# Performance work log

Hardware: AMD Instinct MI355X
Metric: run time of the kernel (lower is better)

## Reference

```python
import jax, jax.numpy as jnp
import numpy as np

B, S, LEN = 1024, 64, 48          # batch, max atoms, atoms per molecule
N = B * LEN                        # total nodes = node_mask.sum()
E = 4 * N                          # edges (avg degree ~4)
D = 256                            # input_dim == hidden_dim == d_model == d_ff
H, HD = D // 8, 8                  # num_heads = hidden_dim // 8
L = 3                              # transformer layers
VOCAB = 65


def _ln(z, s, b):
    mu = z.mean(-1, keepdims=True)
    var = ((z - mu) ** 2).mean(-1, keepdims=True)
    return (z - mu) * jax.lax.rsqrt(var + 1e-5) * s + b


def _forward(x_atoms, edge_index, node_mask, emb_table, conv1_w, conv1_b,
             conv2_w, conv2_b, in_w, in_b, attn_w, attn_b, proj_w, proj_b,
             ln1_s, ln1_b, ff1_w, ff1_b, ff2_w, ff2_b, ln2_s, ln2_b):
    n = x_atoms.shape[0]
    src, dst = edge_index[0], edge_index[1]
    # Embedding with max_norm=1 (torch renormalizes accessed rows)
    e = emb_table[x_atoms]
    nrm = jnp.linalg.norm(e, axis=-1, keepdims=True)
    e = e * jnp.minimum(1.0, 1.0 / (nrm + 1e-7))
    # GCN symmetric normalization with self-loops (shared by both convs)
    deg = jax.ops.segment_sum(jnp.ones((src.shape[0],), e.dtype), dst, num_segments=n) + 1.0
    dinv = jax.lax.rsqrt(deg)
    coef = (dinv[src] * dinv[dst])[:, None]       # per-edge norm
    self_coef = (dinv * dinv)[:, None]            # self-loop norm

    def gcn(h, W, b):
        h = h @ W
        agg = jax.ops.segment_sum(h[src] * coef, dst, num_segments=n)
        return agg + h * self_coef + b

    ones = jnp.ones((n, 1), e.dtype)
    pe = jax.nn.relu(gcn(ones, conv1_w, conv1_b))
    pe = gcn(pe, conv2_w, conv2_b)
    x = e + pe
    # masked_scatter into padded [B, S, D] (row-major fill order)
    mflat = node_mask.reshape(-1)
    rank = jnp.clip(jnp.cumsum(mflat) - 1, 0, n - 1)
    padded = jnp.where(mflat[:, None], x[rank], 0.0).reshape(B, S, D)
    # transformer encoder, post-LN, ReLU FFN; mask [B,1,S,1] as in original
    h = padded @ in_w + in_b
    qmask = node_mask[:, None, :, None]
    scale = 1.0 / np.sqrt(HD).astype(np.float32)
    for l in range(L):
        qkv = h @ attn_w[l] + attn_b[l]
        q, k, v = jnp.split(qkv, 3, axis=-1)
        q = q.reshape(B, S, H, HD)
        k = k.reshape(B, S, H, HD)
        v = v.reshape(B, S, H, HD)
        scores = jnp.einsum('bqhd,bkhd->bhqk', q, k) * scale
        scores = jnp.where(qmask, scores, -1e9)
        attn = jax.nn.softmax(scores, axis=-1)
        o = jnp.einsum('bhqk,bkhd->bqhd', attn, v).reshape(B, S, D)
        h = _ln(h + o @ proj_w[l] + proj_b[l], ln1_s[l], ln1_b[l])
        ff = jax.nn.relu(h @ ff1_w[l] + ff1_b[l]) @ ff2_w[l] + ff2_b[l]
        h = _ln(h + ff, ln2_s[l], ln2_b[l])
    return h


def setup_inputs() -> dict:
    key = jax.random.key(0)
    ks = jax.random.split(key, 16)
    x_atoms = jax.random.randint(ks[0], (N,), 0, VOCAB)
    edge_index = jax.random.randint(ks[1], (2, E), 0, N)
    node_mask = jnp.broadcast_to(jnp.arange(S)[None, :] < LEN, (B, S))
    f32 = jnp.float32
    p = lambda k, shp: (jax.random.normal(k, shp, f32) * 0.02)
    return {
        'x_atoms': x_atoms, 'edge_index': edge_index, 'node_mask': node_mask,
        'emb_table': jax.random.normal(ks[2], (VOCAB, D), f32),
        'conv1_w': p(ks[3], (1, D)), 'conv1_b': jnp.zeros((D,), f32),
        'conv2_w': p(ks[4], (D, D)), 'conv2_b': jnp.zeros((D,), f32),
        'in_w': p(ks[5], (D, D)), 'in_b': jnp.zeros((D,), f32),
        'attn_w': p(ks[6], (L, D, 3 * D)), 'attn_b': jnp.zeros((L, 3 * D), f32),
        'proj_w': p(ks[7], (L, D, D)), 'proj_b': jnp.zeros((L, D), f32),
        'ln1_s': jnp.ones((L, D), f32), 'ln1_b': jnp.zeros((L, D), f32),
        'ff1_w': p(ks[8], (L, D, D)), 'ff1_b': jnp.zeros((L, D), f32),
        'ff2_w': p(ks[9], (L, D, D)), 'ff2_b': jnp.zeros((L, D), f32),
        'ln2_s': jnp.ones((L, D), f32), 'ln2_b': jnp.zeros((L, D), f32),
    }


def reference(x_atoms, edge_index, node_mask, emb_table, conv1_w, conv1_b,
              conv2_w, conv2_b, in_w, in_b, attn_w, attn_b, proj_w, proj_b,
              ln1_s, ln1_b, ff1_w, ff1_b, ff2_w, ff2_b, ln2_s, ln2_b):
    return _forward(x_atoms, edge_index, node_mask, emb_table, conv1_w, conv1_b,
                    conv2_w, conv2_b, in_w, in_b, attn_w, attn_b, proj_w, proj_b,
                    ln1_s, ln1_b, ff1_w, ff1_b, ff2_w, ff2_b, ln2_s, ln2_b)
```

## Files before the change

kernel.cpp:

```cpp
#include <hip/hip_runtime.h>
#include <cstdint>
#include <cstddef>

#define B_   1024
#define S_   64
#define LEN_ 48
#define NN   (B_*LEN_)
#define EE   (4*NN)
#define D_   256
#define H_   32
#define HD_  8
#define ROWS (B_*S_)
#define PLANE 16777216

typedef float  f32x4  __attribute__((ext_vector_type(4)));
typedef __bf16 bf16x8 __attribute__((ext_vector_type(8)));

#define AS1(p) ((const __attribute__((address_space(1))) void*)(p))
#define AS3(p) ((__attribute__((address_space(3))) void*)(p))

__device__ __forceinline__ unsigned short f2bf(float f) {
    union { float f; unsigned u; } x; x.f = f;
    unsigned r = x.u + 0x7fffu + ((x.u >> 16) & 1u);
    return (unsigned short)(r >> 16);
}
__device__ __forceinline__ float bf2f(unsigned short h) {
    union { unsigned u; float f; } x; x.u = (unsigned)h << 16; return x.f;
}
__device__ __forceinline__ bf16x8 u4_to_bf8(uint4 u) {
    union { uint4 u; bf16x8 v; } c; c.u = u; return c.v;
}

__global__ void embed_kernel(const int* __restrict__ atoms,
                             const float* __restrict__ table,
                             float* __restrict__ e) {
    int wave = threadIdx.x >> 6, lane = threadIdx.x & 63;
    int row  = blockIdx.x * 4 + wave;
    int a    = atoms[row];
    float4 v = ((const float4*)(table + (size_t)a * D_))[lane];
    float ss = v.x*v.x + v.y*v.y + v.z*v.z + v.w*v.w;
    #pragma unroll
    for (int off = 32; off; off >>= 1) ss += __shfl_xor(ss, off);
    float nrm = sqrtf(ss);
    float sc  = fminf(1.0f, 1.0f / (nrm + 1e-7f));
    v.x *= sc; v.y *= sc; v.z *= sc; v.w *= sc;
    ((float4*)(e + (size_t)row * D_))[lane] = v;
}

__global__ void fill_kernel(const int* __restrict__ ei, int* __restrict__ cur,
                            int* __restrict__ bucket) {
    int e = blockIdx.x * 256 + threadIdx.x;
    if (e < EE) {
        int s = ei[e], d = ei[EE + e];
        int pos = atomicAdd(&cur[d], 1);
        if (pos < 32) bucket[d * 32 + pos] = s;
    }
}

__global__ void dinv_kernel(const int* __restrict__ cur, float* __restrict__ dinv) {
    int i = blockIdx.x * 256 + threadIdx.x;
    if (i < NN) dinv[i] = rsqrtf((float)cur[i] + 1.0f);
}

__global__ void agg1_kernel(const int* __restrict__ ei, const float* __restrict__ dinv,
                            float* __restrict__ agg1) {
    int e = blockIdx.x * 256 + threadIdx.x;
    if (e < EE) {
        int s = ei[e], d = ei[EE + e];
        atomicAdd(&agg1[d], dinv[s] * dinv[d]);
    }
}

__global__ void pe1_kernel(const float* __restrict__ agg1, const float* __restrict__ dinv,
                           const float* __restrict__ w1, const float* __restrict__ b1,
                           unsigned short* __restrict__ pe1) {
    size_t idx = (size_t)blockIdx.x * 256 + threadIdx.x;
    int i = (int)(idx >> 8), d = (int)(idx & 255);
    float c = agg1[i] + dinv[i] * dinv[i];
    pe1[idx] = f2bf(fmaxf(0.0f, w1[d] * c + b1[d]));
}

__global__ void wconv_kernel(const float* __restrict__ conv2_w, const float* __restrict__ in_w,
                             const float* __restrict__ attn_w, const float* __restrict__ proj_w,
                             const float* __restrict__ ff1_w, const float* __restrict__ ff2_w,
                             unsigned short* __restrict__ wt) {
    int z = blockIdx.y;
    int n = blockIdx.x, k = threadIdx.x;
    const float* src; unsigned short* dst; int N = 256;
    if      (z == 0) { src = conv2_w;                       dst = wt; }
    else if (z == 1) { src = in_w;                          dst = wt + 65536; }
    else if (z <  5) { int l = z - 2;  src = attn_w + (size_t)l * 196608; dst = wt + 131072  + (size_t)l * 196608; N = 768; }
    else if (z <  8) { int l = z - 5;  src = proj_w + (size_t)l * 65536;  dst = wt + 720896  + (size_t)l * 65536; }
    else if (z < 11) { int l = z - 8;  src = ff1_w  + (size_t)l * 65536;  dst = wt + 917504  + (size_t)l * 65536; }
    else             { int l = z - 11; src = ff2_w  + (size_t)l * 65536;  dst = wt + 1114112 + (size_t)l * 65536; }
    if (n < N) dst[(size_t)n * 256 + k] = f2bf(src[(size_t)k * N + n]);
}

__global__ __launch_bounds__(256) void gemm2(
        const unsigned short* __restrict__ A, const unsigned short* __restrict__ WT,
        const float* __restrict__ bias, unsigned short* __restrict__ C0,
        float* __restrict__ Cf, const unsigned short* __restrict__ zeros,
        int amode, int cmode, int relu) {
    __shared__ unsigned short As[128 * 64];
    __shared__ unsigned short Ws[128 * 64];
    const int t = threadIdx.x, w = t >> 6, lane = t & 63;
    const int lr = lane & 15, lq = lane >> 4;
    const size_t m0 = (size_t)blockIdx.y * 128;
    const int    n0 = blockIdx.x * 128;
    const int    N  = gridDim.x * 128;
    const int    wr = (w >> 1) * 64, wc = (w & 1) * 64;

    f32x4 acc[4][4];
    #pragma unroll
    for (int mi = 0; mi < 4; mi++)
        #pragma unroll
        for (int tt = 0; tt < 4; tt++) acc[mi][tt] = (f32x4){0.f, 0.f, 0.f, 0.f};

    const int srow = w * 32 + (lane >> 3);
    const int sj   = lane & 7;

    for (int ki = 0; ki < 4; ki++) {
        if (ki) __syncthreads();
        #pragma unroll
        for (int c = 0; c < 4; c++) {
            int row = srow + c * 8;
            {
                int gch = sj ^ (row & 7);
                const unsigned short* g;
                if (amode == 0) {
                    g = A + (m0 + row) * 256 + ki * 64 + gch * 8;
                } else {
                    size_t grow = m0 + row;
                    int s = (int)(grow & 63);
                    g = (s < LEN_) ? (A + ((grow >> 6) * LEN_ + s) * 256 + ki * 64 + gch * 8)
                                   : zeros;
                }
                __builtin_amdgcn_global_load_lds(AS1(g), AS3(As + w * 2048 + c * 512), 16, 0, 0);
            }
            {
                int gch = sj ^ (row & 7);
                const unsigned short* g = WT + (size_t)(n0 + row) * 256 + ki * 64 + gch * 8;
                __builtin_amdgcn_global_load_lds(AS1(g), AS3(Ws + w * 2048 + c * 512), 16, 0, 0);
            }
        }
        __syncthreads();
        #pragma unroll
        for (int ks = 0; ks < 2; ks++) {
            bf16x8 af[4], bf[4];
            #pragma unroll
            for (int mi = 0; mi < 4; mi++) {
                int row = wr + mi * 16 + lr;
                int cs = (ks * 4 + lq) ^ (row & 7);
                af[mi] = *(const bf16x8*)&As[row * 64 + cs * 8];
            }
            #pragma unroll
            for (int tt = 0; tt < 4; tt++) {
                int col = wc + tt * 16 + lr;
                int cs = (ks * 4 + lq) ^ (col & 7);
                bf[tt] = *(const bf16x8*)&Ws[col * 64 + cs * 8];
            }
            #pragma unroll
            for (int mi = 0; mi < 4; mi++)
                #pragma unroll
                for (int tt = 0; tt < 4; tt++)
                    acc[mi][tt] = __builtin_amdgcn_mfma_f32_16x16x32_bf16(af[mi], bf[tt], acc[mi][tt], 0, 0, 0);
        }
    }
    #pragma unroll
    for (int tt = 0; tt < 4; tt++) {
        int c = n0 + wc + tt * 16 + lr;
        float bv = bias ? bias[c] : 0.0f;
        #pragma unroll
        for (int mi = 0; mi < 4; mi++) {
            #pragma unroll
            for (int r = 0; r < 4; r++) {
                size_t grow = m0 + wr + mi * 16 + lq * 4 + r;
                float v = acc[mi][tt][r] + bv;
                if (relu) v = fmaxf(v, 0.0f);
                if (cmode == 0) {
                    C0[grow * (size_t)N + c] = f2bf(v);
                } else if (cmode == 2) {
                    C0[grow * 256 + c] = f2bf(v);
                    Cf[grow * 256 + c] = v;
                } else {
                    int p = c >> 8, h = (c >> 3) & 31, d = c & 7;
                    size_t bb = grow >> 6, s = grow & 63;
                    C0[(size_t)p * PLANE + ((bb * 32 + h) * 64 + s) * 8 + d] = f2bf(v);
                }
            }
        }
    }
}

__global__ void gather_kernel(const float* __restrict__ xbuf, const unsigned short* __restrict__ h2,
                              const int* __restrict__ cur, const int* __restrict__ bucket,
                              const float* __restrict__ dinv, const float* __restrict__ b2,
                              unsigned short* __restrict__ xg) {
    int w = threadIdx.x >> 6, lane = threadIdx.x & 63;
    int i = blockIdx.x * 4 + w;
    float di = dinv[i];
    ushort4 hv = ((const ushort4*)(h2 + (size_t)i * D_))[lane];
    float4  xv = ((const float4*)(xbuf + (size_t)i * D_))[lane];
    float4  bv = ((const float4*)b2)[lane];
    float a0 = xv.x + bf2f(hv.x) * di * di + bv.x;
    float a1 = xv.y + bf2f(hv.y) * di * di + bv.y;
    float a2 = xv.z + bf2f(hv.z) * di * di + bv.z;
    float a3 = xv.w + bf2f(hv.w) * di * di + bv.w;
    int deg = min(cur[i], 32);
    for (int e = 0; e < deg; e++) {
        int s = bucket[i * 32 + e];
        float c = dinv[s] * di;
        ushort4 sv = ((const ushort4*)(h2 + (size_t)s * D_))[lane];
        a0 += bf2f(sv.x) * c;
        a1 += bf2f(sv.y) * c;
        a2 += bf2f(sv.z) * c;
        a3 += bf2f(sv.w) * c;
    }
    ushort4 out;
    out.x = f2bf(a0); out.y = f2bf(a1); out.z = f2bf(a2); out.w = f2bf(a3);
    ((ushort4*)(xg + (size_t)i * D_))[lane] = out;
}

__global__ __launch_bounds__(256) void attn3_kernel(const unsigned short* __restrict__ qkv,
                                                    unsigned short* __restrict__ o) {
    __shared__ unsigned short Pb[4][64 * 64];
    __shared__ unsigned short VTb[4][16 * 64];
    const int b = blockIdx.x;
    const int w = threadIdx.x >> 6, lane = threadIdx.x & 63;
    const int lr = lane & 15, lq = lane >> 4;
    unsigned short* Pw  = Pb[w];
    unsigned short* VTw = VTb[w];
    const uint4* Q4 = (const uint4*)qkv;
    const uint4* K4 = Q4 + PLANE / 8;
    const uint4* V4 = Q4 + 2 * (PLANE / 8);
    const float scale = 0.35355339059327373f;
    const bf16x8 zf = u4_to_bf8(make_uint4(0, 0, 0, 0));

    for (int hh = 0; hh < 8; hh++) {
        const int h = w * 8 + hh;
        const size_t hb = ((size_t)b * 32 + h) * 64;

        {
            uint4 vrow = V4[hb + lane];
            union { uint4 u; unsigned short s[8]; } vu; vu.u = vrow;
            int ch = lane >> 3, jj = lane & 7;
            #pragma unroll
            for (int d = 0; d < 8; d++)
                VTw[d * 64 + (ch ^ (d & 7)) * 8 + jj] = vu.s[d];
        }

        bf16x8 af[4], bf[4];
        #pragma unroll
        for (int mi = 0; mi < 4; mi++)
            af[mi] = (lq == 0) ? u4_to_bf8(Q4[hb + mi * 16 + lr]) : zf;
        #pragma unroll
        for (int ni = 0; ni < 4; ni++)
            bf[ni] = (lq == 0) ? u4_to_bf8(K4[hb + ni * 16 + lr]) : zf;
        f32x4 s[4][4];
        #pragma unroll
        for (int mi = 0; mi < 4; mi++)
            #pragma unroll
            for (int ni = 0; ni < 4; ni++)
                s[mi][ni] = __builtin_amdgcn_mfma_f32_16x16x32_bf16(
                    af[mi], bf[ni], (f32x4){0.f, 0.f, 0.f, 0.f}, 0, 0, 0);
        #pragma unroll
        for (int ni = 0; ni < 4; ni++) s[3][ni] = (f32x4){0.f, 0.f, 0.f, 0.f};

        #pragma unroll
        for (int mi = 0; mi < 4; mi++) {
            float mx[4], sm[4];
            #pragma unroll
            for (int r = 0; r < 4; r++)
                mx[r] = fmaxf(fmaxf(s[mi][0][r], s[mi][1][r]), fmaxf(s[mi][2][r], s[mi][3][r]));
            #pragma unroll
            for (int st = 1; st <= 8; st <<= 1)
                #pragma unroll
                for (int r = 0; r < 4; r++) mx[r] = fmaxf(mx[r], __shfl_xor(mx[r], st));
            #pragma unroll
            for (int ni = 0; ni < 4; ni++)
                #pragma unroll
                for (int r = 0; r < 4; r++)
                    s[mi][ni][r] = __expf((s[mi][ni][r] - mx[r]) * scale);
            #pragma unroll
            for (int r = 0; r < 4; r++)
                sm[r] = (s[mi][0][r] + s[mi][1][r]) + (s[mi][2][r] + s[mi][3][r]);
            #pragma unroll
            for (int st = 1; st <= 8; st <<= 1)
                #pragma unroll
                for (int r = 0; r < 4; r++) sm[r] += __shfl_xor(sm[r], st);
            #pragma unroll
            for (int r = 0; r < 4; r++) sm[r] = 1.0f / sm[r];
            #pragma unroll
            for (int ni = 0; ni < 4; ni++) {
                int ch = ni * 2 + (lr >> 3), jj = lr & 7;
                #pragma unroll
                for (int r = 0; r < 4; r++) {
                    int q = mi * 16 + lq * 4 + r;
                    Pw[q * 64 + (ch ^ (q & 7)) * 8 + jj] = f2bf(s[mi][ni][r] * sm[r]);
                }
            }
        }

        bf16x8 av[2];
        #pragma unroll
        for (int ks = 0; ks < 2; ks++) {
            int cs = (ks * 4 + lq) ^ (lr & 7);
            av[ks] = *(const bf16x8*)&VTw[lr * 64 + cs * 8];
        }
        #pragma unroll
        for (int ni = 0; ni < 4; ni++) {
            f32x4 oa = (f32x4){0.f, 0.f, 0.f, 0.f};
            #pragma unroll
            for (int ks = 0; ks < 2; ks++) {
                int q = ni * 16 + lr;
                int cs = (ks * 4 + lq) ^ (q & 7);
                bf16x8 pb = *(const bf16x8*)&Pw[q * 64 + cs * 8];
                oa = __builtin_amdgcn_mfma_f32_16x16x32_bf16(av[ks], pb, oa, 0, 0, 0);
            }
            if (lq < 2) {
                int q = ni * 16 + lr;
                ushort4 ov;
                ov.x = f2bf(oa[0]); ov.y = f2bf(oa[1]);
                ov.z = f2bf(oa[2]); ov.w = f2bf(oa[3]);
                *(ushort4*)(o + ((size_t)b * 64 + q) * 256 + h * 8 + lq * 4) = ov;
            }
        }
    }
}

__global__ void ln_kernel(const float* __restrict__ resid, const unsigned short* __restrict__ delta,
                          const float* __restrict__ g, const float* __restrict__ bb,
                          float* __restrict__ outF, unsigned short* __restrict__ outB) {
    int wave = threadIdx.x >> 6, lane = threadIdx.x & 63;
    size_t row = (size_t)blockIdx.x * 4 + wave;
    float4 z0 = ((const float4*)(resid + row * D_))[lane];
    ushort4 d0 = ((const ushort4*)(delta + row * D_))[lane];
    float4 z;
    z.x = z0.x + bf2f(d0.x); z.y = z0.y + bf2f(d0.y);
    z.z = z0.z + bf2f(d0.z); z.w = z0.w + bf2f(d0.w);
    float s1 = z.x + z.y + z.z + z.w;
    float s2 = z.x*z.x + z.y*z.y + z.z*z.z + z.w*z.w;
    #pragma unroll
    for (int off = 32; off; off >>= 1) {
        s1 += __shfl_xor(s1, off);
        s2 += __shfl_xor(s2, off);
    }
    float mu  = s1 * (1.0f / 256.0f);
    float var = s2 * (1.0f / 256.0f) - mu * mu;
    float rs  = rsqrtf(var + 1e-5f);
    float4 gg = ((const float4*)g)[lane];
    float4 bv = ((const float4*)bb)[lane];
    float4 r;
    r.x = (z.x - mu) * rs * gg.x + bv.x;
    r.y = (z.y - mu) * rs * gg.y + bv.y;
    r.z = (z.z - mu) * rs * gg.z + bv.z;
    r.w = (z.w - mu) * rs * gg.w + bv.w;
    ((float4*)(outF + row * D_))[lane] = r;
    if (outB) {
        ushort4 hB;
        hB.x = f2bf(r.x); hB.y = f2bf(r.y); hB.z = f2bf(r.z); hB.w = f2bf(r.w);
        ((ushort4*)(outB + row * D_))[lane] = hB;
    }
}

extern "C" void kernel_launch(void* const* d_in, const int* in_sizes, int n_in,
                              void* d_out, int out_size, void* d_ws, size_t ws_size,
                              hipStream_t stream) {
    const int*   x_atoms = (const int*)d_in[0];
    const int*   ei      = (const int*)d_in[1];
    const float* emb     = (const float*)d_in[3];
    const float* conv1_w = (const float*)d_in[4];
    const float* conv1_b = (const float*)d_in[5];
    const float* conv2_w = (const float*)d_in[6];
    const float* conv2_b = (const float*)d_in[7];
    const float* in_w    = (const float*)d_in[8];
    const float* in_b    = (const float*)d_in[9];
    const float* attn_w  = (const float*)d_in[10];
    const float* attn_b  = (const float*)d_in[11];
    const float* proj_w  = (const float*)d_in[12];
    const float* proj_b  = (const float*)d_in[13];
    const float* ln1_s   = (const float*)d_in[14];
    const float* ln1_b   = (const float*)d_in[15];
    const float* ff1_w   = (const float*)d_in[16];
    const float* ff1_b   = (const float*)d_in[17];
    const float* ff2_w   = (const float*)d_in[18];
    const float* ff2_b   = (const float*)d_in[19];
    const float* ln2_s   = (const float*)d_in[20];
    const float* ln2_b   = (const float*)d_in[21];

    char* ws = (char*)d_ws;
    float*          xbuf = (float*)         (ws + 0);
    unsigned short* pe1  = (unsigned short*)(ws + 50331648);
    unsigned short* xg   = (unsigned short*)(ws + 50331648);
    unsigned short* h2   = (unsigned short*)(ws + 75497472);
    unsigned short* Qp   = (unsigned short*)(ws + 0);
    unsigned short* t1   = (unsigned short*)(ws + 33554432);
    unsigned short* t1bf = (unsigned short*)(ws + 0);
    float*          hbuf = (float*)         (ws + 100663296);
    unsigned short* hbf  = (unsigned short*)(ws + 167772160);
    unsigned short* obuf = (unsigned short*)(ws + 167772160);
    int*            bucket=(int*)           (ws + 201326592);
    unsigned short* wt   = (unsigned short*)(ws + 207618048);
    int*            cur  = (int*)           (ws + 210239488);
    float*          dinv = (float*)         (ws + 210436096);
    float*          agg1 = (float*)         (ws + 210632704);
    unsigned short* zpage= (unsigned short*)(ws + 210829312);

    hipMemsetAsync(cur,   0, NN * 4, stream);
    hipMemsetAsync(agg1,  0, NN * 4, stream);
    hipMemsetAsync(zpage, 0, 256, stream);

    wconv_kernel<<<dim3(768, 14), 256, 0, stream>>>(conv2_w, in_w, attn_w, proj_w, ff1_w, ff2_w, wt);

    embed_kernel<<<NN / 4, 256, 0, stream>>>(x_atoms, emb, xbuf);
    fill_kernel<<<EE / 256, 256, 0, stream>>>(ei, cur, bucket);
    dinv_kernel<<<NN / 256, 256, 0, stream>>>(cur, dinv);
    agg1_kernel<<<EE / 256, 256, 0, stream>>>(ei, dinv, agg1);
    pe1_kernel<<<NN, 256, 0, stream>>>(agg1, dinv, conv1_w, conv1_b, pe1);
    gemm2<<<dim3(2, NN / 128), 256, 0, stream>>>(pe1, wt, nullptr, h2, nullptr, zpage, 0, 0, 0);
    gather_kernel<<<NN / 4, 256, 0, stream>>>(xbuf, h2, cur, bucket, dinv, conv2_b, xg);

    gemm2<<<dim3(2, ROWS / 128), 256, 0, stream>>>(xg, wt + 65536, in_b, hbf, hbuf, zpage, 1, 2, 0);

    for (int l = 0; l < 3; l++) {
        gemm2<<<dim3(6, ROWS / 128), 256, 0, stream>>>(
            hbf, wt + 131072 + (size_t)l * 196608, attn_b + (size_t)l * 768,
            Qp, nullptr, zpage, 0, 3, 0);
        attn3_kernel<<<B_, 256, 0, stream>>>(Qp, obuf);
        gemm2<<<dim3(2, ROWS / 128), 256, 0, stream>>>(
            obuf, wt + 720896 + (size_t)l * 65536, proj_b + (size_t)l * D_,
            t1, nullptr, zpage, 0, 0, 0);
        ln_kernel<<<ROWS / 4, 256, 0, stream>>>(
            hbuf, t1, ln1_s + (size_t)l * D_, ln1_b + (size_t)l * D_, hbuf, hbf);
        gemm2<<<dim3(2, ROWS / 128), 256, 0, stream>>>(
            hbf, wt + 917504 + (size_t)l * 65536, ff1_b + (size_t)l * D_,
            t1bf, nullptr, zpage, 0, 0, 1);
        gemm2<<<dim3(2, ROWS / 128), 256, 0, stream>>>(
            t1bf, wt + 1114112 + (size_t)l * 65536, ff2_b + (size_t)l * D_,
            t1, nullptr, zpage, 0, 0, 0);
        if (l == 2) {
            ln_kernel<<<ROWS / 4, 256, 0, stream>>>(
                hbuf, t1, ln2_s + (size_t)l * D_, ln2_b + (size_t)l * D_, (float*)d_out, nullptr);
        } else {
            ln_kernel<<<ROWS / 4, 256, 0, stream>>>(
                hbuf, t1, ln2_s + (size_t)l * D_, ln2_b + (size_t)l * D_, hbuf, hbf);
        }
    }
}
```

Baseline: 1.201 ms.

## Fuse proj+LayerNorm and FFN+LayerNorm kernels, stage GEMM epilogue through LDS

```diff
diff --git a/kernel.cpp b/kernel.cpp
--- a/kernel.cpp
+++ b/kernel.cpp
@@ -100,14 +100,17 @@
         const unsigned short* __restrict__ A, const unsigned short* __restrict__ WT,
         const float* __restrict__ bias, unsigned short* __restrict__ C0,
         float* __restrict__ Cf, const unsigned short* __restrict__ zeros,
-        int amode, int cmode, int relu) {
-    __shared__ unsigned short As[128 * 64];
-    __shared__ unsigned short Ws[128 * 64];
+        int mt, int amode, int cmode, int relu) {
+    __shared__ unsigned short sh[16384];
+    unsigned short* Asm = sh;
+    unsigned short* Wsm = sh + 8192;
     const int t = threadIdx.x, w = t >> 6, lane = t & 63;
     const int lr = lane & 15, lq = lane >> 4;
-    const size_t m0 = (size_t)blockIdx.y * 128;
-    const int    n0 = blockIdx.x * 128;
-    const int    N  = gridDim.x * 128;
+    const int by = blockIdx.x % mt;
+    const int bx = blockIdx.x / mt;
+    const size_t m0 = (size_t)by * 128;
+    const int    n0 = bx * 128;
+    const int    N  = (gridDim.x / mt) * 128;
     const int    wr = (w >> 1) * 64, wc = (w & 1) * 64;
 
     f32x4 acc[4][4];
@@ -135,58 +138,81 @@
                     g = (s < LEN_) ? (A + ((grow >> 6) * LEN_ + s) * 256 + ki * 64 + gch * 8)
                                    : zeros;
                 }
-                __builtin_amdgcn_global_load_lds(AS1(g), AS3(As + w * 2048 + c * 512), 16, 0, 0);
+                __builtin_amdgcn_global_load_lds(AS1(g), AS3(Asm + w * 2048 + c * 512), 16, 0, 0);
             }
             {
                 int gch = sj ^ (row & 7);
                 const unsigned short* g = WT + (size_t)(n0 + row) * 256 + ki * 64 + gch * 8;
-                __builtin_amdgcn_global_load_lds(AS1(g), AS3(Ws + w * 2048 + c * 512), 16, 0, 0);
+                __builtin_amdgcn_global_load_lds(AS1(g), AS3(Wsm + w * 2048 + c * 512), 16, 0, 0);
             }
         }
         __syncthreads();
         #pragma unroll
         for (int ks = 0; ks < 2; ks++) {
-            bf16x8 af[4], bf[4];
+            bf16x8 af[4], bfr[4];
             #pragma unroll
             for (int mi = 0; mi < 4; mi++) {
                 int row = wr + mi * 16 + lr;
                 int cs = (ks * 4 + lq) ^ (row & 7);
-                af[mi] = *(const bf16x8*)&As[row * 64 + cs * 8];
+                af[mi] = *(const bf16x8*)&Asm[row * 64 + cs * 8];
             }
             #pragma unroll
             for (int tt = 0; tt < 4; tt++) {
                 int col = wc + tt * 16 + lr;
                 int cs = (ks * 4 + lq) ^ (col & 7);
-                bf[tt] = *(const bf16x8*)&Ws[col * 64 + cs * 8];
+                bfr[tt] = *(const bf16x8*)&Wsm[col * 64 + cs * 8];
             }
             #pragma unroll
             for (int mi = 0; mi < 4; mi++)
                 #pragma unroll
                 for (int tt = 0; tt < 4; tt++)
-                    acc[mi][tt] = __builtin_amdgcn_mfma_f32_16x16x32_bf16(af[mi], bf[tt], acc[mi][tt], 0, 0, 0);
-        }
-    }
-    #pragma unroll
-    for (int tt = 0; tt < 4; tt++) {
-        int c = n0 + wc + tt * 16 + lr;
-        float bv = bias ? bias[c] : 0.0f;
-        #pragma unroll
-        for (int mi = 0; mi < 4; mi++) {
-            #pragma unroll
-            for (int r = 0; r < 4; r++) {
-                size_t grow = m0 + wr + mi * 16 + lq * 4 + r;
-                float v = acc[mi][tt][r] + bv;
-                if (relu) v = fmaxf(v, 0.0f);
-                if (cmode == 0) {
-                    C0[grow * (size_t)N + c] = f2bf(v);
-                } else if (cmode == 2) {
+                    acc[mi][tt] = __builtin_amdgcn_mfma_f32_16x16x32_bf16(af[mi], bfr[tt], acc[mi][tt], 0, 0, 0);
+        }
+    }
+    if (cmode == 2) {
+        #pragma unroll
+        for (int tt = 0; tt < 4; tt++) {
+            int c = n0 + wc + tt * 16 + lr;
+            float bv = bias ? bias[c] : 0.0f;
+            #pragma unroll
+            for (int mi = 0; mi < 4; mi++)
+                #pragma unroll
+                for (int r = 0; r < 4; r++) {
+                    size_t grow = m0 + wr + mi * 16 + lq * 4 + r;
+                    float v = acc[mi][tt][r] + bv;
                     C0[grow * 256 + c] = f2bf(v);
                     Cf[grow * 256 + c] = v;
-                } else {
-                    int p = c >> 8, h = (c >> 3) & 31, d = c & 7;
-                    size_t bb = grow >> 6, s = grow & 63;
-                    C0[(size_t)p * PLANE + ((bb * 32 + h) * 64 + s) * 8 + d] = f2bf(v);
                 }
+        }
+    } else {
+        __syncthreads();
+        #pragma unroll
+        for (int tt = 0; tt < 4; tt++) {
+            int col = wc + tt * 16 + lr;
+            float bv = bias ? bias[n0 + col] : 0.0f;
+            #pragma unroll
+            for (int mi = 0; mi < 4; mi++)
+                #pragma unroll
+                for (int r = 0; r < 4; r++) {
+                    int row = wr + mi * 16 + lq * 4 + r;
+                    float v = acc[mi][tt][r] + bv;
+                    if (relu) v = fmaxf(v, 0.0f);
+                    sh[row * 128 + (((col >> 3) ^ (row & 15)) << 3) + (col & 7)] = f2bf(v);
+                }
+        }
+        __syncthreads();
+        #pragma unroll
+        for (int i = 0; i < 8; i++) {
+            int id = i * 256 + t;
+            int row = id >> 4, hch = id & 15;
+            uint4 val = *(const uint4*)&sh[row * 128 + ((hch ^ (row & 15)) << 3)];
+            size_t grow = m0 + row;
+            int c0 = n0 + hch * 8;
+            if (cmode == 0) {
+                *(uint4*)&C0[grow * (size_t)N + c0] = val;
+            } else {
+                int p = c0 >> 8, h = (c0 >> 3) & 31;
+                *(uint4*)&C0[(size_t)p * PLANE + ((grow >> 6) * 32 + h) * 512 + (grow & 63) * 8] = val;
             }
         }
     }
@@ -221,8 +247,7 @@
     ((ushort4*)(xg + (size_t)i * D_))[lane] = out;
 }
 
-__global__ __launch_bounds__(256) void attn3_kernel(const unsigned short* __restrict__ qkv,
-                                                    unsigned short* __restrict__ o) {
+__global__ __launch_bounds__(256) void attn3_kernel(unsigned short* __restrict__ qkv) {
     __shared__ unsigned short Pb[4][64 * 64];
     __shared__ unsigned short VTb[4][16 * 64];
     const int b = blockIdx.x;
@@ -233,6 +258,7 @@
     const uint4* Q4 = (const uint4*)qkv;
     const uint4* K4 = Q4 + PLANE / 8;
     const uint4* V4 = Q4 + 2 * (PLANE / 8);
+    unsigned short* o = qkv;
     const float scale = 0.35355339059327373f;
     const bf16x8 zf = u4_to_bf8(make_uint4(0, 0, 0, 0));
 
@@ -249,20 +275,20 @@
                 VTw[d * 64 + (ch ^ (d & 7)) * 8 + jj] = vu.s[d];
         }
 
-        bf16x8 af[4], bf[4];
+        bf16x8 af[4], bfk[4];
         #pragma unroll
         for (int mi = 0; mi < 4; mi++)
             af[mi] = (lq == 0) ? u4_to_bf8(Q4[hb + mi * 16 + lr]) : zf;
         #pragma unroll
         for (int ni = 0; ni < 4; ni++)
-            bf[ni] = (lq == 0) ? u4_to_bf8(K4[hb + ni * 16 + lr]) : zf;
+            bfk[ni] = (lq == 0) ? u4_to_bf8(K4[hb + ni * 16 + lr]) : zf;
         f32x4 s[4][4];
         #pragma unroll
         for (int mi = 0; mi < 4; mi++)
             #pragma unroll
             for (int ni = 0; ni < 4; ni++)
                 s[mi][ni] = __builtin_amdgcn_mfma_f32_16x16x32_bf16(
-                    af[mi], bf[ni], (f32x4){0.f, 0.f, 0.f, 0.f}, 0, 0, 0);
+                    af[mi], bfk[ni], (f32x4){0.f, 0.f, 0.f, 0.f}, 0, 0, 0);
         #pragma unroll
         for (int ni = 0; ni < 4; ni++) s[3][ni] = (f32x4){0.f, 0.f, 0.f, 0.f};
 
@@ -322,44 +348,205 @@
                 ushort4 ov;
                 ov.x = f2bf(oa[0]); ov.y = f2bf(oa[1]);
                 ov.z = f2bf(oa[2]); ov.w = f2bf(oa[3]);
-                *(ushort4*)(o + ((size_t)b * 64 + q) * 256 + h * 8 + lq * 4) = ov;
-            }
-        }
-    }
-}
-
-__global__ void ln_kernel(const float* __restrict__ resid, const unsigned short* __restrict__ delta,
-                          const float* __restrict__ g, const float* __restrict__ bb,
-                          float* __restrict__ outF, unsigned short* __restrict__ outB) {
-    int wave = threadIdx.x >> 6, lane = threadIdx.x & 63;
-    size_t row = (size_t)blockIdx.x * 4 + wave;
-    float4 z0 = ((const float4*)(resid + row * D_))[lane];
-    ushort4 d0 = ((const ushort4*)(delta + row * D_))[lane];
-    float4 z;
-    z.x = z0.x + bf2f(d0.x); z.y = z0.y + bf2f(d0.y);
-    z.z = z0.z + bf2f(d0.z); z.w = z0.w + bf2f(d0.w);
-    float s1 = z.x + z.y + z.z + z.w;
-    float s2 = z.x*z.x + z.y*z.y + z.z*z.z + z.w*z.w;
-    #pragma unroll
-    for (int off = 32; off; off >>= 1) {
-        s1 += __shfl_xor(s1, off);
-        s2 += __shfl_xor(s2, off);
-    }
-    float mu  = s1 * (1.0f / 256.0f);
-    float var = s2 * (1.0f / 256.0f) - mu * mu;
-    float rs  = rsqrtf(var + 1e-5f);
-    float4 gg = ((const float4*)g)[lane];
-    float4 bv = ((const float4*)bb)[lane];
-    float4 r;
-    r.x = (z.x - mu) * rs * gg.x + bv.x;
-    r.y = (z.y - mu) * rs * gg.y + bv.y;
-    r.z = (z.z - mu) * rs * gg.z + bv.z;
-    r.w = (z.w - mu) * rs * gg.w + bv.w;
-    ((float4*)(outF + row * D_))[lane] = r;
-    if (outB) {
-        ushort4 hB;
-        hB.x = f2bf(r.x); hB.y = f2bf(r.y); hB.z = f2bf(r.z); hB.w = f2bf(r.w);
-        ((ushort4*)(outB + row * D_))[lane] = hB;
+                *(ushort4*)(o + (hb + q) * 8 + lq * 4) = ov;
+            }
+        }
+    }
+}
+
+__global__ __launch_bounds__(256) void projln_kernel(
+        const unsigned short* __restrict__ A, const unsigned short* __restrict__ WT,
+        const float* __restrict__ bias, const float* __restrict__ resid,
+        const float* __restrict__ g, const float* __restrict__ bb,
+        float* __restrict__ outF, unsigned short* __restrict__ outB, int aplane) {
+    __shared__ unsigned short Asm[64 * 64];
+    __shared__ unsigned short Wsm[256 * 64];
+    const int t = threadIdx.x, w = t >> 6, lane = t & 63;
+    const int lr = lane & 15, lq = lane >> 4;
+    const size_t m0 = (size_t)blockIdx.x * 64;
+    f32x4 acc[16];
+    #pragma unroll
+    for (int tt = 0; tt < 16; tt++) acc[tt] = (f32x4){0.f, 0.f, 0.f, 0.f};
+
+    for (int ki = 0; ki < 4; ki++) {
+        if (ki) __syncthreads();
+        #pragma unroll
+        for (int c = 0; c < 2; c++) {
+            int rowl = w * 16 + (lane >> 3) + c * 8;
+            int gch = (lane & 7) ^ (rowl & 7);
+            const unsigned short* gsrc = aplane
+                ? A + (((size_t)blockIdx.x * 32 + ki * 8 + gch) * 64 + rowl) * 8
+                : A + (m0 + rowl) * 256 + ki * 64 + gch * 8;
+            __builtin_amdgcn_global_load_lds(AS1(gsrc), AS3(Asm + w * 1024 + c * 512), 16, 0, 0);
+        }
+        #pragma unroll
+        for (int c = 0; c < 8; c++) {
+            int row = w * 64 + (lane >> 3) + c * 8;
+            const unsigned short* gsrc = WT + (size_t)row * 256 + ki * 64 + ((lane & 7) ^ (row & 7)) * 8;
+            __builtin_amdgcn_global_load_lds(AS1(gsrc), AS3(Wsm + w * 4096 + c * 512), 16, 0, 0);
+        }
+        __syncthreads();
+        #pragma unroll
+        for (int ks = 0; ks < 2; ks++) {
+            int cs = ((ks * 4 + lq) ^ (lr & 7)) << 3;
+            int ra = w * 16 + lr;
+            bf16x8 af = *(const bf16x8*)&Asm[ra * 64 + cs];
+            #pragma unroll
+            for (int tt = 0; tt < 16; tt++) {
+                int col = tt * 16 + lr;
+                bf16x8 bfr = *(const bf16x8*)&Wsm[col * 64 + cs];
+                acc[tt] = __builtin_amdgcn_mfma_f32_16x16x32_bf16(af, bfr, acc[tt], 0, 0, 0);
+            }
+        }
+    }
+    float s1[4] = {0.f,0.f,0.f,0.f}, s2[4] = {0.f,0.f,0.f,0.f};
+    #pragma unroll
+    for (int tt = 0; tt < 16; tt++) {
+        int col = tt * 16 + lr;
+        float bv = bias[col];
+        #pragma unroll
+        for (int r = 0; r < 4; r++) {
+            size_t grow = m0 + w * 16 + lq * 4 + r;
+            float z = acc[tt][r] + bv + resid[grow * 256 + col];
+            acc[tt][r] = z;
+            s1[r] += z; s2[r] += z * z;
+        }
+    }
+    #pragma unroll
+    for (int st = 1; st <= 8; st <<= 1)
+        #pragma unroll
+        for (int r = 0; r < 4; r++) { s1[r] += __shfl_xor(s1[r], st); s2[r] += __shfl_xor(s2[r], st); }
+    float mu[4], rs[4];
+    #pragma unroll
+    for (int r = 0; r < 4; r++) {
+        mu[r] = s1[r] * (1.0f / 256.0f);
+        float var = s2[r] * (1.0f / 256.0f) - mu[r] * mu[r];
+        rs[r] = rsqrtf(var + 1e-5f);
+    }
+    #pragma unroll
+    for (int tt = 0; tt < 16; tt++) {
+        int col = tt * 16 + lr;
+        float gv = g[col], bv2 = bb[col];
+        #pragma unroll
+        for (int r = 0; r < 4; r++) {
+            size_t grow = m0 + w * 16 + lq * 4 + r;
+            float v = (acc[tt][r] - mu[r]) * rs[r] * gv + bv2;
+            outF[grow * 256 + col] = v;
+            outB[grow * 256 + col] = f2bf(v);
+        }
+    }
+}
+
+__global__ __launch_bounds__(256) void ffn_kernel(
+        const unsigned short* __restrict__ A,
+        const unsigned short* __restrict__ W1T, const float* __restrict__ b1,
+        const unsigned short* __restrict__ W2T, const float* __restrict__ b2,
+        const float* __restrict__ resid,
+        const float* __restrict__ g, const float* __restrict__ bb,
+        float* __restrict__ outF, unsigned short* __restrict__ outB) {
+    __shared__ unsigned short Asm[64 * 32];
+    __shared__ unsigned short Wsm[256 * 32];
+    __shared__ unsigned short T[64 * 256];
+    const int t = threadIdx.x, w = t >> 6, lane = t & 63;
+    const int lr = lane & 15, lq = lane >> 4;
+    const size_t m0 = (size_t)blockIdx.x * 64;
+    f32x4 acc[16];
+    #pragma unroll
+    for (int tt = 0; tt < 16; tt++) acc[tt] = (f32x4){0.f, 0.f, 0.f, 0.f};
+
+    for (int ki = 0; ki < 8; ki++) {
+        if (ki) __syncthreads();
+        {
+            int rowl = w * 16 + (lane >> 2);
+            const unsigned short* gsrc = A + (m0 + rowl) * 256 + ki * 32 + (((lane & 3) ^ (rowl & 3)) << 3);
+            __builtin_amdgcn_global_load_lds(AS1(gsrc), AS3(Asm + w * 512), 16, 0, 0);
+        }
+        #pragma unroll
+        for (int c = 0; c < 4; c++) {
+            int row = w * 64 + c * 16 + (lane >> 2);
+            const unsigned short* gsrc = W1T + (size_t)row * 256 + ki * 32 + (((lane & 3) ^ (row & 3)) << 3);
+            __builtin_amdgcn_global_load_lds(AS1(gsrc), AS3(Wsm + w * 2048 + c * 512), 16, 0, 0);
+        }
+        __syncthreads();
+        int cs = (lq ^ (lr & 3)) << 3;
+        int ra = w * 16 + lr;
+        bf16x8 af = *(const bf16x8*)&Asm[ra * 32 + cs];
+        #pragma unroll
+        for (int tt = 0; tt < 16; tt++) {
+            int col = tt * 16 + lr;
+            bf16x8 bfr = *(const bf16x8*)&Wsm[col * 32 + cs];
+            acc[tt] = __builtin_amdgcn_mfma_f32_16x16x32_bf16(af, bfr, acc[tt], 0, 0, 0);
+        }
+    }
+    #pragma unroll
+    for (int tt = 0; tt < 16; tt++) {
+        int col = tt * 16 + lr;
+        float bv = b1[col];
+        int kig = col >> 5, ch = (col >> 3) & 3, jj = col & 7;
+        #pragma unroll
+        for (int r = 0; r < 4; r++) {
+            int rowl = w * 16 + lq * 4 + r;
+            float v = fmaxf(acc[tt][r] + bv, 0.0f);
+            int pos = ch ^ (rowl & 3) ^ ((rowl >> 2) & 3);
+            T[kig * 2048 + rowl * 32 + pos * 8 + jj] = f2bf(v);
+            acc[tt][r] = 0.0f;
+        }
+    }
+    for (int ki = 0; ki < 8; ki++) {
+        __syncthreads();
+        #pragma unroll
+        for (int c = 0; c < 4; c++) {
+            int row = w * 64 + c * 16 + (lane >> 2);
+            const unsigned short* gsrc = W2T + (size_t)row * 256 + ki * 32 + (((lane & 3) ^ (row & 3)) << 3);
+            __builtin_amdgcn_global_load_lds(AS1(gsrc), AS3(Wsm + w * 2048 + c * 512), 16, 0, 0);
+        }
+        __syncthreads();
+        int ra = w * 16 + lr;
+        int pos = lq ^ (lr & 3) ^ ((lr >> 2) & 3);
+        bf16x8 af = *(const bf16x8*)&T[ki * 2048 + ra * 32 + pos * 8];
+        int cs = (lq ^ (lr & 3)) << 3;
+        #pragma unroll
+        for (int tt = 0; tt < 16; tt++) {
+            int col = tt * 16 + lr;
+            bf16x8 bfr = *(const bf16x8*)&Wsm[col * 32 + cs];
+            acc[tt] = __builtin_amdgcn_mfma_f32_16x16x32_bf16(af, bfr, acc[tt], 0, 0, 0);
+        }
+    }
+    float s1[4] = {0.f,0.f,0.f,0.f}, s2[4] = {0.f,0.f,0.f,0.f};
+    #pragma unroll
+    for (int tt = 0; tt < 16; tt++) {
+        int col = tt * 16 + lr;
+        float bv = b2[col];
+        #pragma unroll
+        for (int r = 0; r < 4; r++) {
+            size_t grow = m0 + w * 16 + lq * 4 + r;
+            float z = acc[tt][r] + bv + resid[grow * 256 + col];
+            acc[tt][r] = z;
+            s1[r] += z; s2[r] += z * z;
+        }
+    }
+    #pragma unroll
+    for (int st = 1; st <= 8; st <<= 1)
+        #pragma unroll
+        for (int r = 0; r < 4; r++) { s1[r] += __shfl_xor(s1[r], st); s2[r] += __shfl_xor(s2[r], st); }
+    float mu[4], rs[4];
+    #pragma unroll
+    for (int r = 0; r < 4; r++) {
+        mu[r] = s1[r] * (1.0f / 256.0f);
+        float var = s2[r] * (1.0f / 256.0f) - mu[r] * mu[r];
+        rs[r] = rsqrtf(var + 1e-5f);
+    }
+    #pragma unroll
+    for (int tt = 0; tt < 16; tt++) {
+        int col = tt * 16 + lr;
+        float gv = g[col], bv2 = bb[col];
+        #pragma unroll
+        for (int r = 0; r < 4; r++) {
+            size_t grow = m0 + w * 16 + lq * 4 + r;
+            float v = (acc[tt][r] - mu[r]) * rs[r] * gv + bv2;
+            outF[grow * 256 + col] = v;
+            if (outB) outB[grow * 256 + col] = f2bf(v);
+        }
     }
 }
 
@@ -394,11 +581,8 @@
     unsigned short* xg   = (unsigned short*)(ws + 50331648);
     unsigned short* h2   = (unsigned short*)(ws + 75497472);
     unsigned short* Qp   = (unsigned short*)(ws + 0);
-    unsigned short* t1   = (unsigned short*)(ws + 33554432);
-    unsigned short* t1bf = (unsigned short*)(ws + 0);
     float*          hbuf = (float*)         (ws + 100663296);
     unsigned short* hbf  = (unsigned short*)(ws + 167772160);
-    unsigned short* obuf = (unsigned short*)(ws + 167772160);
     int*            bucket=(int*)           (ws + 201326592);
     unsigned short* wt   = (unsigned short*)(ws + 207618048);
     int*            cur  = (int*)           (ws + 210239488);
@@ -417,33 +601,23 @@
     dinv_kernel<<<NN / 256, 256, 0, stream>>>(cur, dinv);
     agg1_kernel<<<EE / 256, 256, 0, stream>>>(ei, dinv, agg1);
     pe1_kernel<<<NN, 256, 0, stream>>>(agg1, dinv, conv1_w, conv1_b, pe1);
-    gemm2<<<dim3(2, NN / 128), 256, 0, stream>>>(pe1, wt, nullptr, h2, nullptr, zpage, 0, 0, 0);
+    gemm2<<<768, 256, 0, stream>>>(pe1, wt, nullptr, h2, nullptr, zpage, 384, 0, 0, 0);
     gather_kernel<<<NN / 4, 256, 0, stream>>>(xbuf, h2, cur, bucket, dinv, conv2_b, xg);
 
-    gemm2<<<dim3(2, ROWS / 128), 256, 0, stream>>>(xg, wt + 65536, in_b, hbf, hbuf, zpage, 1, 2, 0);
+    gemm2<<<1024, 256, 0, stream>>>(xg, wt + 65536, in_b, hbf, hbuf, zpage, 512, 1, 2, 0);
 
     for (int l = 0; l < 3; l++) {
-        gemm2<<<dim3(6, ROWS / 128), 256, 0, stream>>>(
+        gemm2<<<3072, 256, 0, stream>>>(
             hbf, wt + 131072 + (size_t)l * 196608, attn_b + (size_t)l * 768,
-            Qp, nullptr, zpage, 0, 3, 0);
-        attn3_kernel<<<B_, 256, 0, stream>>>(Qp, obuf);
-        gemm2<<<dim3(2, ROWS / 128), 256, 0, stream>>>(
-            obuf, wt + 720896 + (size_t)l * 65536, proj_b + (size_t)l * D_,
-            t1, nullptr, zpage, 0, 0, 0);
-        ln_kernel<<<ROWS / 4, 256, 0, stream>>>(
-            hbuf, t1, ln1_s + (size_t)l * D_, ln1_b + (size_t)l * D_, hbuf, hbf);
-        gemm2<<<dim3(2, ROWS / 128), 256, 0, stream>>>(
+            Qp, nullptr, zpage, 512, 0, 3, 0);
+        attn3_kernel<<<B_, 256, 0, stream>>>(Qp);
+        projln_kernel<<<ROWS / 64, 256, 0, stream>>>(
+            Qp, wt + 720896 + (size_t)l * 65536, proj_b + (size_t)l * D_, hbuf,
+            ln1_s + (size_t)l * D_, ln1_b + (size_t)l * D_, hbuf, hbf, 1);
+        ffn_kernel<<<ROWS / 64, 256, 0, stream>>>(
             hbf, wt + 917504 + (size_t)l * 65536, ff1_b + (size_t)l * D_,
-            t1bf, nullptr, zpage, 0, 0, 1);
-        gemm2<<<dim3(2, ROWS / 128), 256, 0, stream>>>(
-            t1bf, wt + 1114112 + (size_t)l * 65536, ff2_b + (size_t)l * D_,
-            t1, nullptr, zpage, 0, 0, 0);
-        if (l == 2) {
-            ln_kernel<<<ROWS / 4, 256, 0, stream>>>(
-                hbuf, t1, ln2_s + (size_t)l * D_, ln2_b + (size_t)l * D_, (float*)d_out, nullptr);
-        } else {
-            ln_kernel<<<ROWS / 4, 256, 0, stream>>>(
-                hbuf, t1, ln2_s + (size_t)l * D_, ln2_b + (size_t)l * D_, hbuf, hbf);
-        }
-    }
-}
+            wt + 1114112 + (size_t)l * 65536, ff2_b + (size_t)l * D_, hbuf,
+            ln2_s + (size_t)l * D_, ln2_b + (size_t)l * D_,
+            (l == 2) ? (float*)d_out : hbuf, (l == 2) ? nullptr : hbf);
+    }
+}
```

Measured after the change: 1.048 ms. 12.7% less time.
